# Optimization experiments

Hardware: AMD Instinct MI355X
Metric: run time of the kernel (lower is better)

## Reference

```python
import jax, jax.numpy as jnp
import numpy as np

IN_F, OUT_F, GRID = 1024, 1024, 8
B = 8192
GRID_LO, GRID_HI = -1.0, 1.0


def setup_inputs() -> dict:
    key = jax.random.key(0)
    k1, k2 = jax.random.split(key)
    x = jax.random.normal(k1, (B, IN_F), dtype=jnp.float32)
    # buffers: grid is linspace expanded over in_features; sigma = 1.5*h
    h = (GRID_HI - GRID_LO) / (GRID - 1)
    grid = jnp.broadcast_to(jnp.linspace(GRID_LO, GRID_HI, GRID, dtype=jnp.float32), (IN_F, GRID))
    sigma = jnp.float32(1.5 * h)
    # params
    scale_base = jnp.ones((IN_F, OUT_F), dtype=jnp.float32)
    scale_spline = jnp.ones((IN_F, OUT_F), dtype=jnp.float32)
    # kaiming_uniform-ish init: bound = sqrt(6/fan_in)/sqrt(1+a^2) approximated by small uniform
    fan_in = IN_F * GRID
    gain = np.sqrt(2.0 / (1.0 + 5.0 * 0.1 * 0.1))
    bound = gain * np.sqrt(3.0 / fan_in)
    spline_weight = jax.random.uniform(k2, (OUT_F, IN_F, GRID), dtype=jnp.float32, minval=-bound, maxval=bound)
    return {"x": x, "scale_base": scale_base, "spline_weight": spline_weight,
            "scale_spline": scale_spline, "grid": grid, "sigma": sigma}


def reference(x, scale_base, spline_weight, scale_spline, grid, sigma):
    # x: [B, I]; grid: [I, G]; spline_weight: [O, I, G]; scales: [I, O]
    base_out = jnp.einsum('bi,io->bo', jax.nn.silu(x), scale_base)
    # RBF bases: exp(-((x - grid)/sigma)^2)  -> [B, I, G]
    bases = jnp.exp(-jnp.square((x[:, :, None] - grid[None, :, :]) / sigma))
    # fused spline contraction (mathematically identical to big,oig->bio then bio,io->bo)
    spline_out = jnp.einsum('big,oig,io->bo', bases, spline_weight, scale_spline)
    return base_out + spline_out
```

## Files before the change

### kernel.cpp

```cpp
#include <hip/hip_runtime.h>


#define BATCH 8192
#define IN_F  1024
#define OUT_F 1024
#define GRID_N 8
#define K2    (IN_F * GRID_N)
#define KTOT  (IN_F + K2)

#define BM 128
#define BN 128
#define BK 64
#define BK8 128

typedef __bf16 bf16x8 __attribute__((ext_vector_type(8)));
typedef float  f32x4  __attribute__((ext_vector_type(4)));
typedef int    int32x8 __attribute__((ext_vector_type(8)));

__device__ __forceinline__ void gl2lds16(const void* g, void* l) {
  __builtin_amdgcn_global_load_lds(
      (const __attribute__((address_space(1))) void*)g,
      (__attribute__((address_space(3))) void*)l, 16, 0, 0);
}

__device__ __forceinline__ void pack_fp8x8(const float* v, int& w0, int& w1) {
  w0 = 0; w1 = 0;
  w0 = __builtin_amdgcn_cvt_pk_fp8_f32(v[0], v[1], w0, false);
  w0 = __builtin_amdgcn_cvt_pk_fp8_f32(v[2], v[3], w0, true);
  w1 = __builtin_amdgcn_cvt_pk_fp8_f32(v[4], v[5], w1, false);
  w1 = __builtin_amdgcn_cvt_pk_fp8_f32(v[6], v[7], w1, true);
}

__global__ __launch_bounds__(256)
void kan_transpose_sb(const float* __restrict__ sb, __bf16* __restrict__ sbT) {
  __shared__ float tile[64][65];
  const int o0 = (blockIdx.x & 15) * 64, k0 = (blockIdx.x >> 4) * 64;
  const int t = threadIdx.x;
  const int r = t >> 4, c4 = (t & 15) * 4;
  #pragma unroll
  for (int it = 0; it < 4; ++it) {
    const int k = k0 + r + it * 16;
    float4 v = *(const float4*)(sb + (size_t)k * OUT_F + o0 + c4);
    tile[r + it * 16][c4 + 0] = v.x; tile[r + it * 16][c4 + 1] = v.y;
    tile[r + it * 16][c4 + 2] = v.z; tile[r + it * 16][c4 + 3] = v.w;
  }
  __syncthreads();
  #pragma unroll
  for (int it = 0; it < 4; ++it) {
    const int ol = r + it * 16;
    union { __bf16 h[4]; uint2 q; } s;
    #pragma unroll
    for (int e = 0; e < 4; ++e) s.h[e] = (__bf16)tile[c4 + e][ol];
    *(uint2*)(sbT + (size_t)(o0 + ol) * IN_F + k0 + c4) = s.q;
  }
}

__global__ __launch_bounds__(256)
void kan_mix(const float* __restrict__ x, const __bf16* __restrict__ sbT,
             const float* __restrict__ sw, const float* __restrict__ ss,
             const float* __restrict__ grid, const float* __restrict__ sigma,
             unsigned char* __restrict__ wbt8, unsigned char* __restrict__ Ab8,
             float* __restrict__ out) {
  __shared__ __bf16 As[BM * BK];
  __shared__ __bf16 Bs[BN * BK];
  const int tid = threadIdx.x;
  const int bx  = blockIdx.x;

  if (bx < 512) {
    const int s  = bx >> 3;
    const int r0 = ((bx & 7) * 8 + (s >> 3)) * BM;
    const int c0 = (s & 7) * BN;
    const int lane = tid & 63, wave = tid >> 6;
    const int wm = wave & 1, wn = wave >> 1;
    const int quad = lane >> 4, l15 = lane & 15;

    int a_off[2][4], b_off[2][4];
    #pragma unroll
    for (int ks = 0; ks < 2; ++ks) {
      const int kc = ks * 4 + quad;
      #pragma unroll
      for (int t4 = 0; t4 < 4; ++t4) {
        const int rowA = wm * 64 + t4 * 16 + l15;
        a_off[ks][t4] = (rowA * 8 + (kc ^ (rowA & 7))) * 8;
        const int rowB = wn * 64 + t4 * 16 + l15;
        b_off[ks][t4] = (rowB * 8 + (kc ^ (rowB & 7))) * 8;
      }
    }
    const __bf16* bSrc[4]; int bDst[4];
    #pragma unroll
    for (int it = 0; it < 4; ++it) {
      const int p16 = it * 256 + tid;
      const int row = p16 >> 3;
      const int kc  = (p16 & 7) ^ (row & 7);
      bSrc[it] = sbT + (size_t)(c0 + row) * IN_F + kc * 8;
      bDst[it] = p16 * 8;
    }
    const int m = tid >> 1, half = tid & 1;
    const float* xrow = x + (size_t)(r0 + m) * IN_F;
    int aw_off[4];
    #pragma unroll
    for (int q = 0; q < 4; ++q)
      aw_off[q] = (m * 8 + ((half * 4 + q) ^ (m & 7))) * 8;

    f32x4 zero; zero[0] = 0.f; zero[1] = 0.f; zero[2] = 0.f; zero[3] = 0.f;
    f32x4 acc[4][4];
    #pragma unroll
    for (int a = 0; a < 4; ++a)
      #pragma unroll
      for (int b = 0; b < 4; ++b) acc[a][b] = zero;

    for (int kb = 0; kb < IN_F; kb += BK) {
      union { __bf16 h[32]; uint4 q[4]; } av;
      const float4* xp = (const float4*)(xrow + kb + half * 32);
      #pragma unroll
      for (int j4 = 0; j4 < 8; ++j4) {
        float4 v = xp[j4];
        float vv[4] = {v.x, v.y, v.z, v.w};
        #pragma unroll
        for (int e = 0; e < 4; ++e)
          av.h[j4 * 4 + e] = (__bf16)(vv[e] / (1.0f + __expf(-vv[e])));
      }
      __syncthreads();
      #pragma unroll
      for (int q = 0; q < 4; ++q)
        *(uint4*)&As[aw_off[q]] = av.q[q];
      #pragma unroll
      for (int it = 0; it < 4; ++it)
        gl2lds16(bSrc[it] + kb, &Bs[bDst[it]]);
      __syncthreads();
      #pragma unroll
      for (int ks = 0; ks < 2; ++ks) {
        bf16x8 af[4], bfv[4];
        #pragma unroll
        for (int t4 = 0; t4 < 4; ++t4) af[t4]  = *(const bf16x8*)&As[a_off[ks][t4]];
        #pragma unroll
        for (int t4 = 0; t4 < 4; ++t4) bfv[t4] = *(const bf16x8*)&Bs[b_off[ks][t4]];
        #pragma unroll
        for (int tm = 0; tm < 4; ++tm)
          #pragma unroll
          for (int tn = 0; tn < 4; ++tn)
            acc[tm][tn] = __builtin_amdgcn_mfma_f32_16x16x32_bf16(
                af[tm], bfv[tn], acc[tm][tn], 0, 0, 0);
      }
    }
    #pragma unroll
    for (int tm = 0; tm < 4; ++tm) {
      const int row = r0 + wm * 64 + tm * 16 + quad * 4;
      #pragma unroll
      for (int tn = 0; tn < 4; ++tn) {
        const int col = c0 + wn * 64 + tn * 16 + l15;
        float* op = out + (size_t)row * OUT_F + col;
        #pragma unroll
        for (int r = 0; r < 4; ++r)
          op[(size_t)r * OUT_F] = acc[tm][tn][r];
      }
    }
  } else if (bx < 4608) {
    const size_t e = ((size_t)(bx - 512) * 256 + tid) * 8;
    const int o = (int)(e >> 13);
    const int j = (int)(e & 8191);
    const int i = j >> 3;
    const float sc = ss[(size_t)i * OUT_F + o];
    float4 a = *(const float4*)(sw + e);
    float4 b = *(const float4*)(sw + e + 4);
    float vv[8] = {a.x * sc, a.y * sc, a.z * sc, a.w * sc,
                   b.x * sc, b.y * sc, b.z * sc, b.w * sc};
    int w0, w1; pack_fp8x8(vv, w0, w1);
    *(int2*)(wbt8 + (size_t)o * K2 + j) = make_int2(w0, w1);
  } else {
    const int b = bx - 4608;
    const float inv_sigma = 1.0f / sigma[0];
    const float* xrow = x + (size_t)b * IN_F;
    unsigned char* arow = Ab8 + (size_t)b * K2;
    #pragma unroll
    for (int it = 0; it < 4; ++it) {
      const int i = tid + it * 256;
      const float u = xrow[i];
      float4 g0 = *(const float4*)(grid + (size_t)i * GRID_N);
      float4 g1 = *(const float4*)(grid + (size_t)i * GRID_N + 4);
      float gg[8] = {g0.x, g0.y, g0.z, g0.w, g1.x, g1.y, g1.z, g1.w};
      float bb[8];
      #pragma unroll
      for (int g = 0; g < GRID_N; ++g) {
        float d = (u - gg[g]) * inv_sigma;
        bb[g] = __expf(-d * d);
      }
      int w0, w1; pack_fp8x8(bb, w0, w1);
      *(int2*)(arow + (size_t)i * GRID_N) = make_int2(w0, w1);
    }
  }
}

__global__ __launch_bounds__(256)
void kan_gemm_spline_fp8(const unsigned char* __restrict__ Ab8,
                         const unsigned char* __restrict__ wbt8,
                         float* __restrict__ out) {
  __shared__ unsigned char As[BM * BK8];
  __shared__ unsigned char Bs[BN * BK8];
  const int tid = threadIdx.x;
  const int bx  = blockIdx.x;
  const int s   = bx >> 3;
  const int r0  = ((bx & 7) * 8 + (s >> 3)) * BM;
  const int c0  = (s & 7) * BN;

  const int lane = tid & 63, wave = tid >> 6;
  const int wm = wave & 1, wn = wave >> 1;
  const int quad = lane >> 4, l15 = lane & 15;

  int a_off[4][2], b_off[4][2];
  #pragma unroll
  for (int t4 = 0; t4 < 4; ++t4) {
    const int rowA = wm * 64 + t4 * 16 + l15;
    const int rowB = wn * 64 + t4 * 16 + l15;
    #pragma unroll
    for (int h = 0; h < 2; ++h) {
      a_off[t4][h] = rowA * BK8 + (((quad * 2 + h) ^ (rowA & 7)) * 16);
      b_off[t4][h] = rowB * BK8 + (((quad * 2 + h) ^ (rowB & 7)) * 16);
    }
  }
  const unsigned char* aSrc[4]; const unsigned char* bSrc[4]; int dstOff[4];
  #pragma unroll
  for (int it = 0; it < 4; ++it) {
    const int p16 = it * 256 + tid;
    const int row = p16 >> 3;
    const int kc  = (p16 & 7) ^ (row & 7);
    aSrc[it] = Ab8  + (size_t)(r0 + row) * K2 + kc * 16;
    bSrc[it] = wbt8 + (size_t)(c0 + row) * K2 + kc * 16;
    dstOff[it] = p16 * 16;
  }

  f32x4 zero; zero[0] = 0.f; zero[1] = 0.f; zero[2] = 0.f; zero[3] = 0.f;
  f32x4 acc[4][4];
  #pragma unroll
  for (int a = 0; a < 4; ++a)
    #pragma unroll
    for (int b = 0; b < 4; ++b) acc[a][b] = zero;

  for (int kb = 0; kb < K2; kb += BK8) {
    __syncthreads();
    #pragma unroll
    for (int it = 0; it < 4; ++it) {
      gl2lds16(aSrc[it] + kb, &As[dstOff[it]]);
      gl2lds16(bSrc[it] + kb, &Bs[dstOff[it]]);
    }
    __syncthreads();
    union frag { int32x8 v; uint4 q[2]; };
    frag af[4], bfv[4];
    #pragma unroll
    for (int t4 = 0; t4 < 4; ++t4) {
      af[t4].q[0]  = *(const uint4*)&As[a_off[t4][0]];
      af[t4].q[1]  = *(const uint4*)&As[a_off[t4][1]];
      bfv[t4].q[0] = *(const uint4*)&Bs[b_off[t4][0]];
      bfv[t4].q[1] = *(const uint4*)&Bs[b_off[t4][1]];
    }
    #pragma unroll
    for (int tm = 0; tm < 4; ++tm)
      #pragma unroll
      for (int tn = 0; tn < 4; ++tn)
        acc[tm][tn] = __builtin_amdgcn_mfma_scale_f32_16x16x128_f8f6f4(
            af[tm].v, bfv[tn].v, acc[tm][tn],
            0 , 0 ,
            0, 0x7F7F7F7F ,
            0, 0x7F7F7F7F );
  }

  #pragma unroll
  for (int tm = 0; tm < 4; ++tm) {
    const int row = r0 + wm * 64 + tm * 16 + quad * 4;
    #pragma unroll
    for (int tn = 0; tn < 4; ++tn) {
      const int col = c0 + wn * 64 + tn * 16 + l15;
      float* op = out + (size_t)row * OUT_F + col;
      #pragma unroll
      for (int r = 0; r < 4; ++r)
        op[(size_t)r * OUT_F] += acc[tm][tn][r];
    }
  }
}

__global__ __launch_bounds__(256)
void kan_prep_w_full(const float* __restrict__ sb, const float* __restrict__ sw,
                     const float* __restrict__ ss, __bf16* __restrict__ wbt) {
  const int t = threadIdx.x;
  if (blockIdx.x < 256) {
    __shared__ float tile[64][65];
    const int o0 = (blockIdx.x & 15) * 64, k0 = (blockIdx.x >> 4) * 64;
    const int r = t >> 4, c4 = (t & 15) * 4;
    #pragma unroll
    for (int it = 0; it < 4; ++it) {
      const int k = k0 + r + it * 16;
      float4 v = *(const float4*)(sb + (size_t)k * OUT_F + o0 + c4);
      tile[r + it * 16][c4 + 0] = v.x; tile[r + it * 16][c4 + 1] = v.y;
      tile[r + it * 16][c4 + 2] = v.z; tile[r + it * 16][c4 + 3] = v.w;
    }
    __syncthreads();
    #pragma unroll
    for (int it = 0; it < 4; ++it) {
      const int ol = r + it * 16;
      union { __bf16 h[4]; uint2 q; } s;
      #pragma unroll
      for (int e = 0; e < 4; ++e) s.h[e] = (__bf16)tile[c4 + e][ol];
      *(uint2*)(wbt + (size_t)(o0 + ol) * KTOT + k0 + c4) = s.q;
    }
  } else {
    const size_t e = ((size_t)(blockIdx.x - 256) * 256 + t) * 8;
    const int o = (int)(e >> 13);
    const int j = (int)(e & 8191);
    const int i = j >> 3;
    const float sc = ss[(size_t)i * OUT_F + o];
    float4 a = *(const float4*)(sw + e);
    float4 b = *(const float4*)(sw + e + 4);
    float vv[8] = {a.x, a.y, a.z, a.w, b.x, b.y, b.z, b.w};
    union { __bf16 h[8]; uint4 q; } s;
    #pragma unroll
    for (int g = 0; g < 8; ++g) s.h[g] = (__bf16)(vv[g] * sc);
    *(uint4*)(wbt + (size_t)o * KTOT + IN_F + j) = s.q;
  }
}

__global__ __launch_bounds__(256, 2)
void kan_gemm_fused(const float* __restrict__ x, const __bf16* __restrict__ wbt,
                    const float* __restrict__ grid, const float* __restrict__ sigma,
                    float* __restrict__ out) {
  __shared__ __bf16 As[BM * BK];
  __shared__ __bf16 Bs[BN * BK];
  __shared__ float  gLds[IN_F * GRID_N];
  const int tid = threadIdx.x;
  const int bx  = blockIdx.x;
  const int c0  = (bx & 7) * BN;
  const int r0  = (bx >> 3) * BM;
  for (int idx = tid; idx < IN_F * GRID_N / 4; idx += 256)
    ((float4*)gLds)[idx] = ((const float4*)grid)[idx];
  const float inv_sigma = 1.0f / sigma[0];
  const int lane = tid & 63, wave = tid >> 6;
  const int wm = wave & 1, wn = wave >> 1;
  const int quad = lane >> 4, l15 = lane & 15;
  f32x4 zero; zero[0] = 0.f; zero[1] = 0.f; zero[2] = 0.f; zero[3] = 0.f;
  f32x4 acc[4][4];
  #pragma unroll
  for (int a = 0; a < 4; ++a)
    #pragma unroll
    for (int b = 0; b < 4; ++b) acc[a][b] = zero;
  const int m = tid >> 1, half = tid & 1;
  const float* xrow = x + (size_t)(r0 + m) * IN_F;
  __syncthreads();
  for (int kb = 0; kb < KTOT; kb += BK) {
    union { __bf16 h[32]; uint4 q[4]; } av;
    if (kb < IN_F) {
      const float4* xp = (const float4*)(xrow + kb + half * 32);
      #pragma unroll
      for (int j4 = 0; j4 < 8; ++j4) {
        float4 v = xp[j4];
        float vv[4] = {v.x, v.y, v.z, v.w};
        #pragma unroll
        for (int e = 0; e < 4; ++e)
          av.h[j4 * 4 + e] = (__bf16)(vv[e] / (1.0f + __expf(-vv[e])));
      }
    } else {
      const int i0 = (kb - IN_F) >> 3;
      float4 xv = *(const float4*)(xrow + i0 + half * 4);
      float xs[4] = {xv.x, xv.y, xv.z, xv.w};
      #pragma unroll
      for (int ii = 0; ii < 4; ++ii) {
        const float u = xs[ii];
        const float* gp = &gLds[(i0 + half * 4 + ii) * GRID_N];
        #pragma unroll
        for (int g = 0; g < GRID_N; ++g) {
          float d = (u - gp[g]) * inv_sigma;
          av.h[ii * 8 + g] = (__bf16)__expf(-d * d);
        }
      }
    }
    __syncthreads();
    {
      uint4* dst = (uint4*)&As[m * BK + half * 32];
      #pragma unroll
      for (int qd = 0; qd < 4; ++qd) dst[qd] = av.q[qd];
    }
    #pragma unroll
    for (int it = 0; it < 4; ++it) {
      const int idx = it * 2048 + tid * 8;
      const int n = idx >> 6, k = idx & 63;
      gl2lds16(wbt + (size_t)(c0 + n) * KTOT + kb + k, &Bs[idx]);
    }
    __syncthreads();
    #pragma unroll
    for (int ks = 0; ks < 2; ++ks) {
      bf16x8 af[4], bfv[4];
      #pragma unroll
      for (int t4 = 0; t4 < 4; ++t4)
        af[t4] = *(const bf16x8*)&As[(wm * 64 + t4 * 16 + l15) * BK + ks * 32 + quad * 8];
      #pragma unroll
      for (int t4 = 0; t4 < 4; ++t4)
        bfv[t4] = *(const bf16x8*)&Bs[(wn * 64 + t4 * 16 + l15) * BK + ks * 32 + quad * 8];
      #pragma unroll
      for (int tm = 0; tm < 4; ++tm)
        #pragma unroll
        for (int tn = 0; tn < 4; ++tn)
          acc[tm][tn] = __builtin_amdgcn_mfma_f32_16x16x32_bf16(
              af[tm], bfv[tn], acc[tm][tn], 0, 0, 0);
    }
  }
  #pragma unroll
  for (int tm = 0; tm < 4; ++tm) {
    const int row = r0 + wm * 64 + tm * 16 + quad * 4;
    #pragma unroll
    for (int tn = 0; tn < 4; ++tn) {
      const int col = c0 + wn * 64 + tn * 16 + l15;
      float* op = out + (size_t)row * OUT_F + col;
      #pragma unroll
      for (int r = 0; r < 4; ++r)
        op[(size_t)r * OUT_F] = acc[tm][tn][r];
    }
  }
}

extern "C" void kernel_launch(void* const* d_in, const int* in_sizes, int n_in,
                              void* d_out, int out_size, void* d_ws, size_t ws_size,
                              hipStream_t stream) {
  const float* x     = (const float*)d_in[0];
  const float* sb    = (const float*)d_in[1];
  const float* sw    = (const float*)d_in[2];
  const float* ss    = (const float*)d_in[3];
  const float* grid  = (const float*)d_in[4];
  const float* sigma = (const float*)d_in[5];
  float* out = (float*)d_out;

  const size_t SBT_BYTES = (size_t)OUT_F * IN_F * 2;
  const size_t WS_BYTES  = (size_t)OUT_F * K2;
  const size_t A_BYTES   = (size_t)BATCH * K2;

  if (ws_size >= SBT_BYTES + WS_BYTES + A_BYTES) {
    __bf16*        sbT  = (__bf16*)d_ws;
    unsigned char* wbt8 = (unsigned char*)d_ws + SBT_BYTES;
    unsigned char* Ab8  = (unsigned char*)d_ws + SBT_BYTES + WS_BYTES;
    kan_transpose_sb<<<dim3(256), dim3(256), 0, stream>>>(sb, sbT);
    kan_mix<<<dim3(512 + 4096 + BATCH), dim3(256), 0, stream>>>(
        x, sbT, sw, ss, grid, sigma, wbt8, Ab8, out);
    kan_gemm_spline_fp8<<<dim3((BATCH / BM) * (OUT_F / BN)), dim3(256), 0, stream>>>(
        Ab8, wbt8, out);
  } else {
    __bf16* wbt = (__bf16*)d_ws;
    kan_prep_w_full<<<dim3(4352), dim3(256), 0, stream>>>(sb, sw, ss, wbt);
    kan_gemm_fused<<<dim3((BATCH / BM) * (OUT_F / BN)), dim3(256), 0, stream>>>(
        x, wbt, grid, sigma, out);
  }
}
```

Measured before the change: 265.3 us.

## Merge base GEMM into spline GEMM and precompute SiLU activations in prep kernel

The separate transpose kernel and the base-path GEMM that ran inside the mix kernel are removed. The prep kernel now does the transpose, the weight fp8 packing, the RBF bases, and a bf16 SiLU(x) buffer. A single GEMM kernel runs the fp8 spline K-loop followed by a bf16 base K-loop into the same accumulators and writes the output once. This drops one launch and the read-modify-write of out. The cost is an extra 16MB workspace buffer for SiLU(x) and a longer serial K-loop per tile.

Result: faster. 223.5 us (-15.8%).

```diff
diff --git a/kernel.cpp b/kernel.cpp
--- a/kernel.cpp
+++ b/kernel.cpp
@@ -32,131 +32,35 @@
 }
 
 __global__ __launch_bounds__(256)
-void kan_transpose_sb(const float* __restrict__ sb, __bf16* __restrict__ sbT) {
-  __shared__ float tile[64][65];
-  const int o0 = (blockIdx.x & 15) * 64, k0 = (blockIdx.x >> 4) * 64;
-  const int t = threadIdx.x;
-  const int r = t >> 4, c4 = (t & 15) * 4;
-  #pragma unroll
-  for (int it = 0; it < 4; ++it) {
-    const int k = k0 + r + it * 16;
-    float4 v = *(const float4*)(sb + (size_t)k * OUT_F + o0 + c4);
-    tile[r + it * 16][c4 + 0] = v.x; tile[r + it * 16][c4 + 1] = v.y;
-    tile[r + it * 16][c4 + 2] = v.z; tile[r + it * 16][c4 + 3] = v.w;
-  }
-  __syncthreads();
-  #pragma unroll
-  for (int it = 0; it < 4; ++it) {
-    const int ol = r + it * 16;
-    union { __bf16 h[4]; uint2 q; } s;
-    #pragma unroll
-    for (int e = 0; e < 4; ++e) s.h[e] = (__bf16)tile[c4 + e][ol];
-    *(uint2*)(sbT + (size_t)(o0 + ol) * IN_F + k0 + c4) = s.q;
-  }
-}
-
-__global__ __launch_bounds__(256)
-void kan_mix(const float* __restrict__ x, const __bf16* __restrict__ sbT,
+void kan_mix(const float* __restrict__ x, const float* __restrict__ sb,
              const float* __restrict__ sw, const float* __restrict__ ss,
              const float* __restrict__ grid, const float* __restrict__ sigma,
-             unsigned char* __restrict__ wbt8, unsigned char* __restrict__ Ab8,
-             float* __restrict__ out) {
-  __shared__ __bf16 As[BM * BK];
-  __shared__ __bf16 Bs[BN * BK];
-  const int tid = threadIdx.x;
-  const int bx  = blockIdx.x;
-
-  if (bx < 512) {
-    const int s  = bx >> 3;
-    const int r0 = ((bx & 7) * 8 + (s >> 3)) * BM;
-    const int c0 = (s & 7) * BN;
-    const int lane = tid & 63, wave = tid >> 6;
-    const int wm = wave & 1, wn = wave >> 1;
-    const int quad = lane >> 4, l15 = lane & 15;
-
-    int a_off[2][4], b_off[2][4];
-    #pragma unroll
-    for (int ks = 0; ks < 2; ++ks) {
-      const int kc = ks * 4 + quad;
-      #pragma unroll
-      for (int t4 = 0; t4 < 4; ++t4) {
-        const int rowA = wm * 64 + t4 * 16 + l15;
-        a_off[ks][t4] = (rowA * 8 + (kc ^ (rowA & 7))) * 8;
-        const int rowB = wn * 64 + t4 * 16 + l15;
-        b_off[ks][t4] = (rowB * 8 + (kc ^ (rowB & 7))) * 8;
-      }
-    }
-    const __bf16* bSrc[4]; int bDst[4];
-    #pragma unroll
-    for (int it = 0; it < 4; ++it) {
-      const int p16 = it * 256 + tid;
-      const int row = p16 >> 3;
-      const int kc  = (p16 & 7) ^ (row & 7);
-      bSrc[it] = sbT + (size_t)(c0 + row) * IN_F + kc * 8;
-      bDst[it] = p16 * 8;
-    }
-    const int m = tid >> 1, half = tid & 1;
-    const float* xrow = x + (size_t)(r0 + m) * IN_F;
-    int aw_off[4];
-    #pragma unroll
-    for (int q = 0; q < 4; ++q)
-      aw_off[q] = (m * 8 + ((half * 4 + q) ^ (m & 7))) * 8;
-
-    f32x4 zero; zero[0] = 0.f; zero[1] = 0.f; zero[2] = 0.f; zero[3] = 0.f;
-    f32x4 acc[4][4];
-    #pragma unroll
-    for (int a = 0; a < 4; ++a)
-      #pragma unroll
-      for (int b = 0; b < 4; ++b) acc[a][b] = zero;
-
-    for (int kb = 0; kb < IN_F; kb += BK) {
-      union { __bf16 h[32]; uint4 q[4]; } av;
-      const float4* xp = (const float4*)(xrow + kb + half * 32);
-      #pragma unroll
-      for (int j4 = 0; j4 < 8; ++j4) {
-        float4 v = xp[j4];
-        float vv[4] = {v.x, v.y, v.z, v.w};
-        #pragma unroll
-        for (int e = 0; e < 4; ++e)
-          av.h[j4 * 4 + e] = (__bf16)(vv[e] / (1.0f + __expf(-vv[e])));
-      }
-      __syncthreads();
-      #pragma unroll
-      for (int q = 0; q < 4; ++q)
-        *(uint4*)&As[aw_off[q]] = av.q[q];
-      #pragma unroll
-      for (int it = 0; it < 4; ++it)
-        gl2lds16(bSrc[it] + kb, &Bs[bDst[it]]);
-      __syncthreads();
-      #pragma unroll
-      for (int ks = 0; ks < 2; ++ks) {
-        bf16x8 af[4], bfv[4];
-        #pragma unroll
-        for (int t4 = 0; t4 < 4; ++t4) af[t4]  = *(const bf16x8*)&As[a_off[ks][t4]];
-        #pragma unroll
-        for (int t4 = 0; t4 < 4; ++t4) bfv[t4] = *(const bf16x8*)&Bs[b_off[ks][t4]];
-        #pragma unroll
-        for (int tm = 0; tm < 4; ++tm)
-          #pragma unroll
-          for (int tn = 0; tn < 4; ++tn)
-            acc[tm][tn] = __builtin_amdgcn_mfma_f32_16x16x32_bf16(
-                af[tm], bfv[tn], acc[tm][tn], 0, 0, 0);
-      }
-    }
-    #pragma unroll
-    for (int tm = 0; tm < 4; ++tm) {
-      const int row = r0 + wm * 64 + tm * 16 + quad * 4;
-      #pragma unroll
-      for (int tn = 0; tn < 4; ++tn) {
-        const int col = c0 + wn * 64 + tn * 16 + l15;
-        float* op = out + (size_t)row * OUT_F + col;
-        #pragma unroll
-        for (int r = 0; r < 4; ++r)
-          op[(size_t)r * OUT_F] = acc[tm][tn][r];
-      }
-    }
-  } else if (bx < 4608) {
-    const size_t e = ((size_t)(bx - 512) * 256 + tid) * 8;
+             __bf16* __restrict__ sbT, unsigned char* __restrict__ wbt8,
+             unsigned char* __restrict__ Ab8, __bf16* __restrict__ sbA) {
+  const int t = threadIdx.x;
+  const int bx = blockIdx.x;
+  if (bx < 256) {
+    __shared__ float tile[64][65];
+    const int o0 = (bx & 15) * 64, k0 = (bx >> 4) * 64;
+    const int r = t >> 4, c4 = (t & 15) * 4;
+    #pragma unroll
+    for (int it = 0; it < 4; ++it) {
+      const int k = k0 + r + it * 16;
+      float4 v = *(const float4*)(sb + (size_t)k * OUT_F + o0 + c4);
+      tile[r + it * 16][c4 + 0] = v.x; tile[r + it * 16][c4 + 1] = v.y;
+      tile[r + it * 16][c4 + 2] = v.z; tile[r + it * 16][c4 + 3] = v.w;
+    }
+    __syncthreads();
+    #pragma unroll
+    for (int it = 0; it < 4; ++it) {
+      const int ol = r + it * 16;
+      union { __bf16 h[4]; uint2 q; } s;
+      #pragma unroll
+      for (int e = 0; e < 4; ++e) s.h[e] = (__bf16)tile[c4 + e][ol];
+      *(uint2*)(sbT + (size_t)(o0 + ol) * IN_F + k0 + c4) = s.q;
+    }
+  } else if (bx < 4352) {
+    const size_t e = ((size_t)(bx - 256) * 256 + t) * 8;
     const int o = (int)(e >> 13);
     const int j = (int)(e & 8191);
     const int i = j >> 3;
@@ -168,13 +72,22 @@
     int w0, w1; pack_fp8x8(vv, w0, w1);
     *(int2*)(wbt8 + (size_t)o * K2 + j) = make_int2(w0, w1);
   } else {
-    const int b = bx - 4608;
+    const int b = bx - 4352;
     const float inv_sigma = 1.0f / sigma[0];
     const float* xrow = x + (size_t)b * IN_F;
     unsigned char* arow = Ab8 + (size_t)b * K2;
-    #pragma unroll
-    for (int it = 0; it < 4; ++it) {
-      const int i = tid + it * 256;
+    __bf16* srow = sbA + (size_t)b * IN_F;
+    {
+      float4 v = ((const float4*)xrow)[t];
+      float vv[4] = {v.x, v.y, v.z, v.w};
+      union { __bf16 h[4]; uint2 q; } s;
+      #pragma unroll
+      for (int e = 0; e < 4; ++e) s.h[e] = (__bf16)(vv[e] / (1.0f + __expf(-vv[e])));
+      ((uint2*)srow)[t] = s.q;
+    }
+    #pragma unroll
+    for (int it = 0; it < 4; ++it) {
+      const int i = t + it * 256;
       const float u = xrow[i];
       float4 g0 = *(const float4*)(grid + (size_t)i * GRID_N);
       float4 g1 = *(const float4*)(grid + (size_t)i * GRID_N + 4);
@@ -192,11 +105,16 @@
 }
 
 __global__ __launch_bounds__(256)
-void kan_gemm_spline_fp8(const unsigned char* __restrict__ Ab8,
-                         const unsigned char* __restrict__ wbt8,
-                         float* __restrict__ out) {
-  __shared__ unsigned char As[BM * BK8];
-  __shared__ unsigned char Bs[BN * BK8];
+void kan_gemm_all(const unsigned char* __restrict__ Ab8,
+                  const unsigned char* __restrict__ wbt8,
+                  const __bf16* __restrict__ sbA,
+                  const __bf16* __restrict__ sbT,
+                  float* __restrict__ out) {
+  __shared__ unsigned char As8[BM * BK8];
+  __shared__ unsigned char Bs8[BN * BK8];
+  __bf16* As16 = (__bf16*)As8;
+  __bf16* Bs16 = (__bf16*)Bs8;
+
   const int tid = threadIdx.x;
   const int bx  = blockIdx.x;
   const int s   = bx >> 3;
@@ -207,26 +125,42 @@
   const int wm = wave & 1, wn = wave >> 1;
   const int quad = lane >> 4, l15 = lane & 15;
 
-  int a_off[4][2], b_off[4][2];
+  int a_off8[4][2], b_off8[4][2];
   #pragma unroll
   for (int t4 = 0; t4 < 4; ++t4) {
     const int rowA = wm * 64 + t4 * 16 + l15;
     const int rowB = wn * 64 + t4 * 16 + l15;
     #pragma unroll
     for (int h = 0; h < 2; ++h) {
-      a_off[t4][h] = rowA * BK8 + (((quad * 2 + h) ^ (rowA & 7)) * 16);
-      b_off[t4][h] = rowB * BK8 + (((quad * 2 + h) ^ (rowB & 7)) * 16);
-    }
-  }
-  const unsigned char* aSrc[4]; const unsigned char* bSrc[4]; int dstOff[4];
+      a_off8[t4][h] = rowA * BK8 + (((quad * 2 + h) ^ (rowA & 7)) * 16);
+      b_off8[t4][h] = rowB * BK8 + (((quad * 2 + h) ^ (rowB & 7)) * 16);
+    }
+  }
+  int a_off16[2][4], b_off16[2][4];
+  #pragma unroll
+  for (int ks = 0; ks < 2; ++ks) {
+    const int kc = ks * 4 + quad;
+    #pragma unroll
+    for (int t4 = 0; t4 < 4; ++t4) {
+      const int rowA = wm * 64 + t4 * 16 + l15;
+      a_off16[ks][t4] = (rowA * 8 + (kc ^ (rowA & 7))) * 8;
+      const int rowB = wn * 64 + t4 * 16 + l15;
+      b_off16[ks][t4] = (rowB * 8 + (kc ^ (rowB & 7))) * 8;
+    }
+  }
+  const int p16 = tid;
+  const unsigned char* aSrc8[4]; const unsigned char* bSrc8[4];
+  const __bf16* aSrc16[4]; const __bf16* bSrc16[4]; int dstOff[4];
   #pragma unroll
   for (int it = 0; it < 4; ++it) {
-    const int p16 = it * 256 + tid;
-    const int row = p16 >> 3;
-    const int kc  = (p16 & 7) ^ (row & 7);
-    aSrc[it] = Ab8  + (size_t)(r0 + row) * K2 + kc * 16;
-    bSrc[it] = wbt8 + (size_t)(c0 + row) * K2 + kc * 16;
-    dstOff[it] = p16 * 16;
+    const int p = it * 256 + p16;
+    const int row = p >> 3;
+    const int kc  = (p & 7) ^ (row & 7);
+    aSrc8[it]  = Ab8  + (size_t)(r0 + row) * K2 + kc * 16;
+    bSrc8[it]  = wbt8 + (size_t)(c0 + row) * K2 + kc * 16;
+    aSrc16[it] = sbA  + (size_t)(r0 + row) * IN_F + kc * 8;
+    bSrc16[it] = sbT  + (size_t)(c0 + row) * IN_F + kc * 8;
+    dstOff[it] = p * 16;
   }
 
   f32x4 zero; zero[0] = 0.f; zero[1] = 0.f; zero[2] = 0.f; zero[3] = 0.f;
@@ -240,18 +174,18 @@
     __syncthreads();
     #pragma unroll
     for (int it = 0; it < 4; ++it) {
-      gl2lds16(aSrc[it] + kb, &As[dstOff[it]]);
-      gl2lds16(bSrc[it] + kb, &Bs[dstOff[it]]);
+      gl2lds16(aSrc8[it] + kb, &As8[dstOff[it]]);
+      gl2lds16(bSrc8[it] + kb, &Bs8[dstOff[it]]);
     }
     __syncthreads();
     union frag { int32x8 v; uint4 q[2]; };
     frag af[4], bfv[4];
     #pragma unroll
     for (int t4 = 0; t4 < 4; ++t4) {
-      af[t4].q[0]  = *(const uint4*)&As[a_off[t4][0]];
-      af[t4].q[1]  = *(const uint4*)&As[a_off[t4][1]];
-      bfv[t4].q[0] = *(const uint4*)&Bs[b_off[t4][0]];
-      bfv[t4].q[1] = *(const uint4*)&Bs[b_off[t4][1]];
+      af[t4].q[0]  = *(const uint4*)&As8[a_off8[t4][0]];
+      af[t4].q[1]  = *(const uint4*)&As8[a_off8[t4][1]];
+      bfv[t4].q[0] = *(const uint4*)&Bs8[b_off8[t4][0]];
+      bfv[t4].q[1] = *(const uint4*)&Bs8[b_off8[t4][1]];
     }
     #pragma unroll
     for (int tm = 0; tm < 4; ++tm)
@@ -259,9 +193,31 @@
       for (int tn = 0; tn < 4; ++tn)
         acc[tm][tn] = __builtin_amdgcn_mfma_scale_f32_16x16x128_f8f6f4(
             af[tm].v, bfv[tn].v, acc[tm][tn],
-            0 , 0 ,
-            0, 0x7F7F7F7F ,
-            0, 0x7F7F7F7F );
+            0, 0, 0, 0x7F7F7F7F, 0, 0x7F7F7F7F);
+  }
+
+  for (int kb = 0; kb < IN_F; kb += BK) {
+    __syncthreads();
+    #pragma unroll
+    for (int it = 0; it < 4; ++it) {
+      gl2lds16(aSrc16[it] + kb, (char*)As16 + dstOff[it]);
+      gl2lds16(bSrc16[it] + kb, (char*)Bs16 + dstOff[it]);
+    }
+    __syncthreads();
+    #pragma unroll
+    for (int ks = 0; ks < 2; ++ks) {
+      bf16x8 af[4], bfv[4];
+      #pragma unroll
+      for (int t4 = 0; t4 < 4; ++t4) af[t4]  = *(const bf16x8*)&As16[a_off16[ks][t4]];
+      #pragma unroll
+      for (int t4 = 0; t4 < 4; ++t4) bfv[t4] = *(const bf16x8*)&Bs16[b_off16[ks][t4]];
+      #pragma unroll
+      for (int tm = 0; tm < 4; ++tm)
+        #pragma unroll
+        for (int tn = 0; tn < 4; ++tn)
+          acc[tm][tn] = __builtin_amdgcn_mfma_f32_16x16x32_bf16(
+              af[tm], bfv[tn], acc[tm][tn], 0, 0, 0);
+    }
   }
 
   #pragma unroll
@@ -273,7 +229,7 @@
       float* op = out + (size_t)row * OUT_F + col;
       #pragma unroll
       for (int r = 0; r < 4; ++r)
-        op[(size_t)r * OUT_F] += acc[tm][tn][r];
+        op[(size_t)r * OUT_F] = acc[tm][tn][r];
     }
   }
 }
@@ -429,16 +385,17 @@
   const size_t SBT_BYTES = (size_t)OUT_F * IN_F * 2;
   const size_t WS_BYTES  = (size_t)OUT_F * K2;
   const size_t A_BYTES   = (size_t)BATCH * K2;
-
-  if (ws_size >= SBT_BYTES + WS_BYTES + A_BYTES) {
+  const size_t SBA_BYTES = (size_t)BATCH * IN_F * 2;
+
+  if (ws_size >= SBT_BYTES + WS_BYTES + A_BYTES + SBA_BYTES) {
     __bf16*        sbT  = (__bf16*)d_ws;
     unsigned char* wbt8 = (unsigned char*)d_ws + SBT_BYTES;
     unsigned char* Ab8  = (unsigned char*)d_ws + SBT_BYTES + WS_BYTES;
-    kan_transpose_sb<<<dim3(256), dim3(256), 0, stream>>>(sb, sbT);
-    kan_mix<<<dim3(512 + 4096 + BATCH), dim3(256), 0, stream>>>(
-        x, sbT, sw, ss, grid, sigma, wbt8, Ab8, out);
-    kan_gemm_spline_fp8<<<dim3((BATCH / BM) * (OUT_F / BN)), dim3(256), 0, stream>>>(
-        Ab8, wbt8, out);
+    __bf16*        sbA  = (__bf16*)((char*)d_ws + SBT_BYTES + WS_BYTES + A_BYTES);
+    kan_mix<<<dim3(4352 + BATCH), dim3(256), 0, stream>>>(
+        x, sb, sw, ss, grid, sigma, sbT, wbt8, Ab8, sbA);
+    kan_gemm_all<<<dim3((BATCH / BM) * (OUT_F / BN)), dim3(256), 0, stream>>>(
+        Ab8, wbt8, sbA, sbT, out);
   } else {
     __bf16* wbt = (__bf16*)d_ws;
     kan_prep_w_full<<<dim3(4352), dim3(256), 0, stream>>>(sb, sw, ss, wbt);
```
